# Performance work log

Hardware: AMD Instinct MI355X
Metric: run time of the kernel (lower is better)

## Reference

```python
import jax, jax.numpy as jnp
import numpy as np

B, S, D = 2, 512, 2048          # batch, seq, hidden
H, Dh = 16, 128                 # heads, head_dim
E, K, G, TG = 8, 2, 2, 1        # experts, top_k, n_group, topk_group
I, IS = 1024, 1024              # routed / shared expert intermediate
ROUTED_SCALE = 2.5
EPS = 1e-6
ROPE_THETA = 10000.0


def setup_inputs() -> dict:
    key = jax.random.key(0)
    ks = jax.random.split(key, 13)
    p = lambda k, shape, s=0.02: jax.random.normal(k, shape, jnp.float32) * s
    return {
        "hidden_states": jax.random.normal(ks[0], (B, S, D), jnp.float32),
        "ln1_w": jnp.ones((D,), jnp.float32),
        "ln2_w": jnp.ones((D,), jnp.float32),
        "wq": p(ks[1], (D, H * Dh)),
        "wk": p(ks[2], (D, H * Dh)),
        "wv": p(ks[3], (D, H * Dh)),
        "wo": p(ks[4], (H * Dh, D)),
        "gate_w": p(ks[5], (E, D)),
        "gate_bias": p(ks[6], (E,), 0.1),
        "w_gate": p(ks[7], (E, D, I)),
        "w_up": p(ks[8], (E, D, I)),
        "w_down": p(ks[9], (E, I, D)),
        "sw_gate": p(ks[10], (D, IS)),
        "sw_up": p(ks[11], (D, IS)),
        "sw_down": p(ks[12], (IS, D)),
    }


def _rmsnorm(x, w):
    var = jnp.mean(x * x, axis=-1, keepdims=True)
    return x * jax.lax.rsqrt(var + EPS) * w


def _rope_cos_sin(seq_len):
    inv_freq = 1.0 / (ROPE_THETA ** (jnp.arange(0, Dh, 2, dtype=jnp.float32) / Dh))
    ang = jnp.arange(seq_len, dtype=jnp.float32)[:, None] * inv_freq  # [S, Dh/2]
    return jnp.cos(ang)[None, :, None, :], jnp.sin(ang)[None, :, None, :]


def _apply_rope(x, cos, sin):
    x1, x2 = jnp.split(x, 2, axis=-1)
    return jnp.concatenate([x1 * cos - x2 * sin, x2 * cos + x1 * sin], axis=-1)


def _attention(x, wq, wk, wv, wo):
    q = (x @ wq).reshape(B, S, H, Dh)
    k = (x @ wk).reshape(B, S, H, Dh)
    v = (x @ wv).reshape(B, S, H, Dh)
    cos, sin = _rope_cos_sin(S)
    q = _apply_rope(q, cos, sin)
    k = _apply_rope(k, cos, sin)
    scores = jnp.einsum('bqhd,bkhd->bhqk', q, k) * (1.0 / np.sqrt(Dh).astype(np.float32))
    causal = jnp.tril(jnp.ones((S, S), bool))
    scores = jnp.where(causal, scores, jnp.finfo(scores.dtype).min)
    attn = jax.nn.softmax(scores, axis=-1)
    out = jnp.einsum('bhqk,bkhd->bqhd', attn, v).reshape(B, S, H * Dh)
    return out @ wo


def _moe(x, gate_w, gate_bias, w_gate, w_up, w_down, sw_gate, sw_up, sw_down):
    # x: [T, D]. noaux_tc grouped top-k routing (DeepSeek-V3 style).
    T = x.shape[0]
    logits = x @ gate_w.T                      # [T, E]
    scores = jax.nn.sigmoid(logits)
    sc = scores + gate_bias                    # selection scores with correction bias
    grp = sc.reshape(T, G, E // G)
    group_scores = jnp.sum(jax.lax.top_k(grp, 2)[0], axis=-1)  # top-2 sum per group [T,G]
    _, gidx = jax.lax.top_k(group_scores, TG)
    gmask = jnp.zeros((T, G), bool).at[jnp.arange(T)[:, None], gidx].set(True)
    emask = jnp.broadcast_to(gmask[:, :, None], (T, G, E // G)).reshape(T, E)
    masked = jnp.where(emask, sc, -jnp.inf)
    _, idx = jax.lax.top_k(masked, K)          # [T, K] expert ids
    w = jnp.take_along_axis(scores, idx, axis=-1)
    w = w / jnp.sum(w, axis=-1, keepdims=True)  # norm_topk_prob=True
    # dense combine weights [T, E] (zero except K entries per token)
    cw = jnp.zeros((T, E), x.dtype).at[jnp.arange(T)[:, None], idx].add(w)

    def body(acc, xs):
        wg, wu, wd, cwe = xs
        y = (jax.nn.silu(x @ wg) * (x @ wu)) @ wd  # SiluAndMul gated MLP
        return acc + cwe[:, None] * y, None

    routed, _ = jax.lax.scan(body, jnp.zeros_like(x), (w_gate, w_up, w_down, cw.T))
    shared = (jax.nn.silu(x @ sw_gate) * (x @ sw_up)) @ sw_down
    return routed * ROUTED_SCALE + shared


def reference(hidden_states, ln1_w, ln2_w, wq, wk, wv, wo, gate_w, gate_bias,
              w_gate, w_up, w_down, sw_gate, sw_up, sw_down):
    h = hidden_states
    h = h + _attention(_rmsnorm(h, ln1_w), wq, wk, wv, wo)
    x = _rmsnorm(h, ln2_w).reshape(B * S, D)
    moe_out = _moe(x, gate_w, gate_bias, w_gate, w_up, w_down,
                   sw_gate, sw_up, sw_down).reshape(B, S, D)
    return h + moe_out
```

## Files before the change

kernel.cpp:

```cpp
#include <hip/hip_runtime.h>

typedef __bf16 bf16x4 __attribute__((ext_vector_type(4)));
typedef __bf16 bf16x8 __attribute__((ext_vector_type(8)));
typedef float  f32x4  __attribute__((ext_vector_type(4)));

#define THREADS 256
constexpr int BK = 32, BKP = 40;

constexpr size_t MB = 1024*1024;
constexpr size_t oH2    = 0;
constexpr size_t oXB2   = 8*MB;
constexpr size_t oRT    = 12*MB;
constexpr size_t oWQKVT = 16*MB;
constexpr size_t oWQKVL = 40*MB;
constexpr size_t oWOT   = 64*MB;
constexpr size_t oWOL   = 72*MB;
constexpr size_t oXN1   = 80*MB;
constexpr size_t oXN1L  = 84*MB;
constexpr size_t oQKV   = 88*MB;
constexpr size_t oSCF   = 112*MB;
constexpr size_t oQKS   = 144*MB;
constexpr size_t oQKSL  = 152*MB;
constexpr size_t oVT    = 16*MB;
constexpr size_t oVTL   = 20*MB;
constexpr size_t oATT   = 24*MB;
constexpr size_t oPB    = 40*MB;
constexpr size_t oPBL2  = 88*MB;
constexpr size_t oWGUT  = 16*MB;
constexpr size_t oWDT   = 80*MB;
constexpr size_t oSGUT  = 112*MB;
constexpr size_t oSDT   = 120*MB;
constexpr size_t oGU    = 124*MB;
constexpr size_t oHB    = 140*MB;
constexpr size_t oY     = 144*MB;
constexpr size_t oSGU   = 16*MB;
constexpr size_t oSHB   = 24*MB;
constexpr size_t oSDB   = 26*MB;
constexpr size_t oEIDX = oRT;
constexpr size_t oEW   = oRT + 8192;
constexpr size_t oSLOT = oRT + 16384;
constexpr size_t oLIST = oRT + 24576;
constexpr size_t oCNT  = oRT + 32768;
constexpr size_t oOFF  = oRT + 33024;
constexpr size_t oCUR  = oRT + 33280;

__device__ __forceinline__ bf16x8 bzero8() {
  bf16x8 z;
#pragma unroll
  for (int j = 0; j < 8; ++j) z[j] = (__bf16)0.f;
  return z;
}

template<int OM>
__global__ void transpose_kernel(const float* __restrict__ in, __bf16* __restrict__ out,
                                 int ldin, int ldout, int zlo,
                                 long inBH, long inBL, long outB, long plane) {
  __shared__ float tile[64][65];
  int z = blockIdx.z;
  const float* inp = in + (long)(z / zlo) * inBH + (long)(z % zlo) * inBL;
  __bf16* outp = out + (long)z * outB;
  int r0 = blockIdx.y * 64, c0 = blockIdx.x * 64;
  int tid = threadIdx.x;
#pragma unroll
  for (int i = 0; i < 4; ++i) {
    int lin = tid + i * 256;
    int r = lin >> 4, c4 = (lin & 15) << 2;
    f32x4 v = *(const f32x4*)(inp + (long)(r0 + r) * ldin + c0 + c4);
    tile[r][c4] = v[0]; tile[r][c4+1] = v[1]; tile[r][c4+2] = v[2]; tile[r][c4+3] = v[3];
  }
  __syncthreads();
#pragma unroll
  for (int i = 0; i < 4; ++i) {
    int lin = tid + i * 256;
    int oR = lin >> 4, oC4 = (lin & 15) << 2;
    bf16x4 hi, lo;
#pragma unroll
    for (int j = 0; j < 4; ++j) {
      float v = tile[oC4 + j][oR];
      hi[j] = (__bf16)v;
      if constexpr (OM == 2) lo[j] = (__bf16)(v - (float)hi[j]);
    }
    __bf16* dst = outp + (long)(c0 + oR) * ldout + r0 + oC4;
    *(bf16x4*)dst = hi;
    if constexpr (OM == 2) *(bf16x4*)(dst + plane) = lo;
  }
}

template<int MODE, int SP, bool RESID, bool CAUSAL, bool KTRI, int TBM = 128, int TBN = 128>
__global__ __launch_bounds__(256, 2)
void gemm_kernel(const void* __restrict__ Av, const void* __restrict__ Bv, float* __restrict__ C,
                 const float* __restrict__ Rres,
                 int M, int N, int K, int lda, int ldb, int ldc,
                 int zlo, long aHi, long aLo, long bHi, long bLo, long cHi, long cLo,
                 long aPlane, long bPlane,
                 const int* __restrict__ counts, const int* __restrict__ offsets,
                 const int* __restrict__ gather) {
  const int n0 = blockIdx.x * TBN;
  const int m0 = blockIdx.y * TBM;
  const int z  = blockIdx.z;
  if (CAUSAL && n0 > m0) return;

  const float*  Af = (const float*)Av;
  const __bf16* Ah = (const __bf16*)Av;
  const __bf16* Bh = (const __bf16*)Bv;

  int mcount; int rowbase = 0;
  long aoff = 0, boff = 0, coff = 0;
  if constexpr (MODE == 0) {
    mcount = M;
    int zh = z / zlo, zl = z % zlo;
    aoff = (long)zh*aHi + (long)zl*aLo;
    boff = (long)zh*bHi + (long)zl*bLo;
    coff = (long)zh*cHi + (long)zl*cLo;
  } else {
    mcount = counts[z];
    rowbase = offsets[z];
    if (m0 >= mcount) return;
    boff = (long)z*bHi;
  }

  constexpr bool TRI = (SP != 0);
  constexpr int ABUF = TBM*BKP;
  constexpr int BBUF = TBN*BKP;
  constexpr int WTM = TBM/2, WTN = TBN/2;
  constexpr int MI = WTM/16, MJ = WTN/16;
  __shared__ __align__(16) __bf16 As[(TRI?2:1)*ABUF];
  __shared__ __align__(16) __bf16 Bs[(TRI?2:1)*BBUF];

  const int tid = threadIdx.x;
  const int lane = tid & 63, wave = tid >> 6;
  const int wm = wave >> 1, wn = wave & 1;
  const int lq = lane >> 4, lr = lane & 15;

  int kend = K;
  if (KTRI) { int ke = m0 + TBM; kend = ke < K ? ke : K; }

  f32x4 acc[MI][MJ] = {};

  for (int k0 = 0; k0 < kend; k0 += BK) {
    if (k0) __syncthreads();
    if constexpr (SP == 1) {
#pragma unroll
      for (int it = 0; it < TBM/32; ++it) {
        int lin = tid + it*THREADS;
        int row = lin >> 3;
        int c4  = (lin & 7) << 2;
        int gr  = m0 + row;
        bf16x4 hi, lo;
#pragma unroll
        for (int j = 0; j < 4; ++j) { hi[j]=(__bf16)0.f; lo[j]=(__bf16)0.f; }
        if (gr < mcount) {
          long arow = gr;
          f32x4 v = *(const f32x4*)(Af + aoff + arow*(long)lda + k0 + c4);
#pragma unroll
          for (int j = 0; j < 4; ++j) {
            hi[j] = (__bf16)v[j];
            lo[j] = (__bf16)(v[j] - (float)hi[j]);
          }
        }
        *(bf16x4*)(As + row*BKP + c4) = hi;
        *(bf16x4*)(As + ABUF + row*BKP + c4) = lo;
      }
    } else {
#pragma unroll
      for (int it = 0; it < TBM/64; ++it) {
        int lin = tid + it*THREADS;
        int row = lin >> 2;
        int c8  = (lin & 3) << 3;
        int gr  = m0 + row;
        bf16x8 hi = bzero8(), lo;
        if constexpr (SP == 2) lo = bzero8();
        if (gr < mcount) {
          long arow;
          if constexpr (MODE == 1) arow = gather[rowbase + gr];
          else if constexpr (MODE == 2) arow = rowbase + gr;
          else arow = gr;
          const __bf16* p = Ah + aoff + arow*(long)lda + k0 + c8;
          hi = *(const bf16x8*)p;
          if constexpr (SP == 2) lo = *(const bf16x8*)(p + aPlane);
        }
        *(bf16x8*)(As + row*BKP + c8) = hi;
        if constexpr (SP == 2) *(bf16x8*)(As + ABUF + row*BKP + c8) = lo;
      }
    }
#pragma unroll
    for (int it = 0; it < TBN/64; ++it) {
      int lin = tid + it*THREADS;
      int row = lin >> 2;
      int c8  = (lin & 3) << 3;
      const __bf16* p = Bh + boff + (long)(n0+row)*ldb + k0 + c8;
      *(bf16x8*)(Bs + row*BKP + c8) = *(const bf16x8*)p;
      if constexpr (TRI) *(bf16x8*)(Bs + BBUF + row*BKP + c8) = *(const bf16x8*)(p + bPlane);
    }
    __syncthreads();

    bf16x8 fa[MI], fal[MI];
    const __bf16* ap = As + (wm*WTM + lr)*BKP + lq*8;
    const __bf16* bp = Bs + (wn*WTN + lr)*BKP + lq*8;
#pragma unroll
    for (int i = 0; i < MI; ++i) {
      fa[i] = *(const bf16x8*)(ap + i*16*BKP);
      if constexpr (TRI) fal[i] = *(const bf16x8*)(ap + ABUF + i*16*BKP);
    }
#pragma unroll
    for (int j = 0; j < MJ; ++j) {
      bf16x8 fb = *(const bf16x8*)(bp + j*16*BKP);
      if constexpr (TRI) {
        bf16x8 fbl = *(const bf16x8*)(bp + BBUF + j*16*BKP);
#pragma unroll
        for (int i = 0; i < MI; ++i) {
          acc[i][j] = __builtin_amdgcn_mfma_f32_16x16x32_bf16(fa[i],  fbl, acc[i][j], 0, 0, 0);
          acc[i][j] = __builtin_amdgcn_mfma_f32_16x16x32_bf16(fal[i], fb,  acc[i][j], 0, 0, 0);
          acc[i][j] = __builtin_amdgcn_mfma_f32_16x16x32_bf16(fa[i],  fb,  acc[i][j], 0, 0, 0);
        }
      } else {
#pragma unroll
        for (int i = 0; i < MI; ++i)
          acc[i][j] = __builtin_amdgcn_mfma_f32_16x16x32_bf16(fa[i], fb, acc[i][j], 0, 0, 0);
      }
    }
  }

#pragma unroll
  for (int i = 0; i < MI; ++i) {
#pragma unroll
    for (int rg = 0; rg < 4; ++rg) {
      int lrow = wm*WTM + i*16 + lq*4 + rg;
      int gr = m0 + lrow;
      if (gr < mcount) {
        long crow = coff + (long)(rowbase + gr)*ldc;
#pragma unroll
        for (int j = 0; j < MJ; ++j) {
          int col = n0 + wn*WTN + j*16 + lr;
          float val = acc[i][j][rg];
          if constexpr (RESID) val += Rres[(long)gr*ldc + col];
          C[crow + col] = val;
        }
      }
    }
  }
}

template<int OM>
__global__ void rmsnorm_kernel(const float* __restrict__ x, const float* __restrict__ w,
                               __bf16* __restrict__ out, long plane) {
  const int row = blockIdx.x;
  const float* xr = x + (long)row * 2048;
  float ss = 0.f;
  for (int d = threadIdx.x; d < 2048; d += 256) { float v = xr[d]; ss += v*v; }
  __shared__ float red[4];
  int lane = threadIdx.x & 63, wave = threadIdx.x >> 6;
#pragma unroll
  for (int off = 32; off; off >>= 1) ss += __shfl_down(ss, off, 64);
  if (lane == 0) red[wave] = ss;
  __syncthreads();
  float tot = red[0] + red[1] + red[2] + red[3];
  float rs = rsqrtf(tot * (1.f/2048.f) + 1e-6f);
  __bf16* orow = out + (long)row * 2048;
  for (int d = threadIdx.x; d < 2048; d += 256) {
    float v = xr[d]*rs*w[d];
    __bf16 h = (__bf16)v;
    orow[d] = h;
    if constexpr (OM == 2) orow[d + plane] = (__bf16)(v - (float)h);
  }
}

__global__ void rope_split_kernel(const float* __restrict__ qkv, __bf16* __restrict__ o, long plane) {
  int tid = blockIdx.x*256 + threadIdx.x;
  int i = tid & 63;
  int th = tid >> 6;
  int h = th & 15;
  int t = th >> 4;
  int s = t & 511;
  long ib = (long)t*6144 + h*128;
  long ob = (long)t*4096 + h*128;
  float inv = 1.f / powf(10000.f, (float)i * (1.f/64.f));
  float ang = (float)s * inv;
  float c = cosf(ang), sn = sinf(ang);
  float q1 = qkv[ib+i], q2 = qkv[ib+64+i];
  float r1 = q1*c - q2*sn, r2 = q2*c + q1*sn;
  __bf16 h1 = (__bf16)r1, h2v = (__bf16)r2;
  o[ob+i] = h1;            o[ob+i+plane] = (__bf16)(r1 - (float)h1);
  o[ob+64+i] = h2v;        o[ob+64+i+plane] = (__bf16)(r2 - (float)h2v);
  float k1 = qkv[ib+2048+i], k2 = qkv[ib+2048+64+i];
  float s1 = k1*c - k2*sn, s2 = k2*c + k1*sn;
  __bf16 g1 = (__bf16)s1, g2 = (__bf16)s2;
  o[ob+2048+i] = g1;       o[ob+2048+i+plane] = (__bf16)(s1 - (float)g1);
  o[ob+2048+64+i] = g2;    o[ob+2048+64+i+plane] = (__bf16)(s2 - (float)g2);
}

__global__ void softmax_kernel(const float* __restrict__ sc, __bf16* __restrict__ p, long plane) {
  int r = blockIdx.x & 511;
  long bh = blockIdx.x >> 9;
  const float scale = 0.08838834764831845f;
  long base = (bh*512 + r)*512;
  int c0 = threadIdx.x, c1 = threadIdx.x + 256;
  float v0 = (c0 <= r) ? sc[base+c0]*scale : -3.0e38f;
  float v1 = (c1 <= r) ? sc[base+c1]*scale : -3.0e38f;
  float m = fmaxf(v0, v1);
  __shared__ float red[4];
  int lane = threadIdx.x & 63, wave = threadIdx.x >> 6;
#pragma unroll
  for (int off = 32; off; off >>= 1) m = fmaxf(m, __shfl_xor(m, off, 64));
  if (lane == 0) red[wave] = m;
  __syncthreads();
  m = fmaxf(fmaxf(red[0], red[1]), fmaxf(red[2], red[3]));
  __syncthreads();
  float e0 = (c0 <= r) ? expf(v0 - m) : 0.f;
  float e1 = (c1 <= r) ? expf(v1 - m) : 0.f;
  float s = e0 + e1;
#pragma unroll
  for (int off = 32; off; off >>= 1) s += __shfl_xor(s, off, 64);
  if (lane == 0) red[wave] = s;
  __syncthreads();
  s = red[0] + red[1] + red[2] + red[3];
  float inv = 1.f / s;
  float p0 = e0*inv, p1 = e1*inv;
  __bf16 h0 = (__bf16)p0, h1 = (__bf16)p1;
  p[base+c0] = h0; p[base+c0+plane] = (__bf16)(p0 - (float)h0);
  p[base+c1] = h1; p[base+c1+plane] = (__bf16)(p1 - (float)h1);
}

__global__ void zero8_kernel(int* c) { if (threadIdx.x < 8) c[threadIdx.x] = 0; }

__global__ void routing_kernel(const float* __restrict__ h2, const float* __restrict__ ln2w,
                               const float* __restrict__ gw, const float* __restrict__ gb,
                               int* __restrict__ eidx, float* __restrict__ ew,
                               int* __restrict__ counts) {
  int t = blockIdx.x;
  const float* xr = h2 + (long)t*2048;
  int lane = threadIdx.x & 63, wave = threadIdx.x >> 6;
  float ss = 0.f;
  for (int d = threadIdx.x; d < 2048; d += 256) { float v = xr[d]; ss += v*v; }
  __shared__ float red[4];
#pragma unroll
  for (int off = 32; off; off >>= 1) ss += __shfl_down(ss, off, 64);
  if (lane == 0) red[wave] = ss;
  __syncthreads();
  float rs = rsqrtf((red[0]+red[1]+red[2]+red[3]) * (1.f/2048.f) + 1e-6f);
  __shared__ float lg[8];
  for (int e = wave; e < 8; e += 4) {
    const float* wr = gw + (long)e*2048;
    float acc = 0.f;
    for (int d = lane; d < 2048; d += 64) acc += (xr[d]*rs*ln2w[d]) * wr[d];
#pragma unroll
    for (int off = 32; off; off >>= 1) acc += __shfl_down(acc, off, 64);
    if (lane == 0) lg[e] = acc;
  }
  __syncthreads();
  if (threadIdx.x == 0) {
    float sg[8], sc[8];
#pragma unroll
    for (int e = 0; e < 8; ++e) { sg[e] = 1.f/(1.f+expf(-lg[e])); sc[e] = sg[e] + gb[e]; }
    float gs[2];
#pragma unroll
    for (int g = 0; g < 2; ++g) {
      float m1 = -3e38f, m2 = -3e38f;
#pragma unroll
      for (int j = 0; j < 4; ++j) {
        float v = sc[4*g+j];
        if (v > m1) { m2 = m1; m1 = v; } else if (v > m2) m2 = v;
      }
      gs[g] = m1 + m2;
    }
    int b4 = (gs[1] > gs[0]) ? 4 : 0;
    int i1 = 0; float v1 = -3e38f;
#pragma unroll
    for (int j = 0; j < 4; ++j) if (sc[b4+j] > v1) { v1 = sc[b4+j]; i1 = j; }
    int i2 = -1; float v2 = -3e38f;
#pragma unroll
    for (int j = 0; j < 4; ++j) if (j != i1 && sc[b4+j] > v2) { v2 = sc[b4+j]; i2 = j; }
    float w1 = sg[b4+i1], w2 = sg[b4+i2], s = w1 + w2;
    eidx[t*2] = b4+i1; eidx[t*2+1] = b4+i2;
    ew[t*2] = w1/s;    ew[t*2+1] = w2/s;
    atomicAdd(&counts[b4+i1], 1); atomicAdd(&counts[b4+i2], 1);
  }
}

__global__ void scan_kernel(const int* __restrict__ counts, int* __restrict__ offsets,
                            int* __restrict__ cursors) {
  if (threadIdx.x == 0 && blockIdx.x == 0) {
    int s = 0;
    for (int e = 0; e < 8; ++e) { offsets[e] = s; s += counts[e]; cursors[e] = 0; }
    offsets[8] = s;
  }
}

__global__ void scatter_kernel(const int* __restrict__ eidx, const int* __restrict__ offsets,
                               int* __restrict__ cursors, int* __restrict__ list,
                               int* __restrict__ slot) {
  int t = blockIdx.x*256 + threadIdx.x;
  if (t < 1024) {
#pragma unroll
    for (int kk = 0; kk < 2; ++kk) {
      int e = eidx[t*2+kk];
      int pos = atomicAdd(&cursors[e], 1);
      int g = offsets[e] + pos;
      list[g] = t;
      slot[t*2+kk] = g;
    }
  }
}

__global__ void silumul_kernel(const float* __restrict__ gu, __bf16* __restrict__ o, int n) {
  int i = blockIdx.x*256 + threadIdx.x;
  if (i < n) {
    int s = i >> 10, j = i & 1023;
    float gv = gu[(long)s*2048 + j];
    float uv = gu[(long)s*2048 + 1024 + j];
    float sg = gv / (1.f + expf(-gv));
    o[i] = (__bf16)(sg * uv);
  }
}

__global__ void combine_kernel(const float* __restrict__ h2, const float* __restrict__ y,
                               const float* __restrict__ sdown, const int* __restrict__ slot,
                               const float* __restrict__ ew, float* __restrict__ out) {
  int i = blockIdx.x*256 + threadIdx.x;
  int t = i >> 11;
  int d = i & 2047;
  float rv = ew[t*2]   * y[(long)slot[t*2]  *2048 + d]
           + ew[t*2+1] * y[(long)slot[t*2+1]*2048 + d];
  out[i] = h2[i] + sdown[i] + 2.5f * rv;
}

extern "C" void kernel_launch(void* const* d_in, const int* in_sizes, int n_in,
                              void* d_out, int out_size, void* d_ws, size_t ws_size,
                              hipStream_t stream) {
  const float* hid  = (const float*)d_in[0];
  const float* ln1  = (const float*)d_in[1];
  const float* ln2  = (const float*)d_in[2];
  const float* wq   = (const float*)d_in[3];
  const float* wk   = (const float*)d_in[4];
  const float* wv   = (const float*)d_in[5];
  const float* wo   = (const float*)d_in[6];
  const float* gw   = (const float*)d_in[7];
  const float* gb   = (const float*)d_in[8];
  const float* wgat = (const float*)d_in[9];
  const float* wup  = (const float*)d_in[10];
  const float* wdn  = (const float*)d_in[11];
  const float* swg  = (const float*)d_in[12];
  const float* swu  = (const float*)d_in[13];
  const float* swd  = (const float*)d_in[14];
  float* out = (float*)d_out;
  char* ws = (char*)d_ws;

  float*  h2    = (float*)(ws + oH2);
  __bf16* xb2   = (__bf16*)(ws + oXB2);
  __bf16* wqkvT = (__bf16*)(ws + oWQKVT);
  __bf16* woT   = (__bf16*)(ws + oWOT);
  __bf16* xn1   = (__bf16*)(ws + oXN1);
  float*  qkv   = (float*)(ws + oQKV);
  float*  scf   = (float*)(ws + oSCF);
  __bf16* qks   = (__bf16*)(ws + oQKS);
  __bf16* vtb   = (__bf16*)(ws + oVT);
  float*  att   = (float*)(ws + oATT);
  __bf16* pb    = (__bf16*)(ws + oPB);
  __bf16* wgut  = (__bf16*)(ws + oWGUT);
  __bf16* wdt   = (__bf16*)(ws + oWDT);
  __bf16* sgut  = (__bf16*)(ws + oSGUT);
  __bf16* sdt   = (__bf16*)(ws + oSDT);
  float*  gu    = (float*)(ws + oGU);
  __bf16* hb    = (__bf16*)(ws + oHB);
  float*  ybuf  = (float*)(ws + oY);
  float*  sgu   = (float*)(ws + oSGU);
  __bf16* shb   = (__bf16*)(ws + oSHB);
  float*  sdb   = (float*)(ws + oSDB);
  int*   eidx = (int*)(ws + oEIDX);
  float* ew   = (float*)(ws + oEW);
  int*   slot = (int*)(ws + oSLOT);
  int*   list = (int*)(ws + oLIST);
  int*   cnt  = (int*)(ws + oCNT);
  int*   offs = (int*)(ws + oOFF);
  int*   curs = (int*)(ws + oCUR);

  const long S22 = (long)2048*2048, S21 = (long)2048*1024;
  const long pWQKV = (oWQKVL - oWQKVT) / 2;
  const long pWO   = (oWOL - oWOT) / 2;
  const long pXN1  = 2*MB;
  const long pQKS  = (oQKSL - oQKS) / 2;
  const long pVT   = 2*MB;
  const long pPB   = (oPBL2 - oPB) / 2;

  transpose_kernel<2><<<dim3(32,32,1), 256, 0, stream>>>(wq, wqkvT,          2048, 2048, 1, 0, 0, 0, pWQKV);
  transpose_kernel<2><<<dim3(32,32,1), 256, 0, stream>>>(wk, wqkvT + S22,    2048, 2048, 1, 0, 0, 0, pWQKV);
  transpose_kernel<2><<<dim3(32,32,1), 256, 0, stream>>>(wv, wqkvT + 2*S22,  2048, 2048, 1, 0, 0, 0, pWQKV);
  transpose_kernel<2><<<dim3(32,32,1), 256, 0, stream>>>(wo, woT,            2048, 2048, 1, 0, 0, 0, pWO);

  rmsnorm_kernel<2><<<1024, 256, 0, stream>>>(hid, ln1, xn1, pXN1);

  gemm_kernel<0, 2, false, false, false, 64, 128><<<dim3(48,16,1), 256, 0, stream>>>(
      xn1, wqkvT, qkv, nullptr, 1024, 6144, 2048, 2048, 2048, 6144,
      1, 0, 0, 0, 0, 0, 0, pXN1, pWQKV, nullptr, nullptr, nullptr);

  rope_split_kernel<<<4096, 256, 0, stream>>>(qkv, qks, pQKS);

  transpose_kernel<2><<<dim3(2,8,32), 256, 0, stream>>>(
      qkv + 4096, vtb, 6144, 512, 16, (long)512*6144, 128, (long)128*512, pVT);

  gemm_kernel<0, 2, false, true, false, 64, 64><<<dim3(8,8,32), 256, 0, stream>>>(
      qks, qks + 2048, scf, nullptr, 512, 512, 128, 4096, 4096, 512,
      16, (long)512*4096, 128, (long)512*4096, 128, (long)16*512*512, (long)512*512,
      pQKS, pQKS, nullptr, nullptr, nullptr);

  softmax_kernel<<<16384, 256, 0, stream>>>(scf, pb, pPB);

  gemm_kernel<0, 2, false, false, true, 64, 64><<<dim3(2,8,32), 256, 0, stream>>>(
      pb, vtb, att, nullptr, 512, 128, 512, 512, 512, 2048,
      16, (long)16*512*512, (long)512*512, (long)16*128*512, (long)128*512,
      (long)512*2048, 128, pPB, pVT, nullptr, nullptr, nullptr);

  gemm_kernel<0, 1, true, false, false, 64, 64><<<dim3(32,16,1), 256, 0, stream>>>(
      att, woT, h2, hid, 1024, 2048, 2048, 2048, 2048, 2048,
      1, 0, 0, 0, 0, 0, 0, 0, pWO, nullptr, nullptr, nullptr);

  rmsnorm_kernel<1><<<1024, 256, 0, stream>>>(h2, ln2, xb2, 0);
  zero8_kernel<<<1, 64, 0, stream>>>(cnt);
  routing_kernel<<<1024, 256, 0, stream>>>(h2, ln2, gw, gb, eidx, ew, cnt);
  scan_kernel<<<1, 64, 0, stream>>>(cnt, offs, curs);
  scatter_kernel<<<4, 256, 0, stream>>>(eidx, offs, curs, list, slot);

  transpose_kernel<1><<<dim3(16,32,8), 256, 0, stream>>>(wgat, wgut,        1024, 2048, 1, S21, 0, S22, 0);
  transpose_kernel<1><<<dim3(16,32,8), 256, 0, stream>>>(wup,  wgut + S21,  1024, 2048, 1, S21, 0, S22, 0);
  transpose_kernel<1><<<dim3(32,16,8), 256, 0, stream>>>(wdn,  wdt,         2048, 1024, 1, S21, 0, S21, 0);
  transpose_kernel<1><<<dim3(16,32,1), 256, 0, stream>>>(swg,  sgut,        1024, 2048, 1, 0, 0, 0, 0);
  transpose_kernel<1><<<dim3(16,32,1), 256, 0, stream>>>(swu,  sgut + S21,  1024, 2048, 1, 0, 0, 0, 0);
  transpose_kernel<1><<<dim3(32,16,1), 256, 0, stream>>>(swd,  sdt,         2048, 1024, 1, 0, 0, 0, 0);

  gemm_kernel<1, 0, false, false, false, 64, 64><<<dim3(32,16,8), 256, 0, stream>>>(
      xb2, wgut, gu, nullptr, 1024, 2048, 2048, 2048, 2048, 2048,
      1, 0, 0, S22, 0, 0, 0, 0, 0, cnt, offs, list);
  silumul_kernel<<<8192, 256, 0, stream>>>(gu, hb, 2048*1024);
  gemm_kernel<2, 0, false, false, false, 64, 64><<<dim3(32,16,8), 256, 0, stream>>>(
      hb, wdt, ybuf, nullptr, 1024, 2048, 1024, 1024, 1024, 2048,
      1, 0, 0, S21, 0, 0, 0, 0, 0, cnt, offs, nullptr);

  gemm_kernel<0, 0, false, false, false, 64, 64><<<dim3(32,16,1), 256, 0, stream>>>(
      xb2, sgut, sgu, nullptr, 1024, 2048, 2048, 2048, 2048, 2048,
      1, 0, 0, 0, 0, 0, 0, 0, 0, nullptr, nullptr, nullptr);
  silumul_kernel<<<4096, 256, 0, stream>>>(sgu, shb, 1024*1024);
  gemm_kernel<0, 0, false, false, false, 64, 64><<<dim3(32,16,1), 256, 0, stream>>>(
      shb, sdt, sdb, nullptr, 1024, 2048, 1024, 1024, 1024, 2048,
      1, 0, 0, 0, 0, 0, 0, 0, 0, nullptr, nullptr, nullptr);

  combine_kernel<<<8192, 256, 0, stream>>>(h2, ybuf, sdb, slot, ew, out);
}
```

Baseline: 812.7 us.

## Double-buffer GEMM shared tiles with register prefetch of next K slice

```diff
diff --git a/kernel.cpp b/kernel.cpp
--- a/kernel.cpp
+++ b/kernel.cpp
@@ -122,10 +122,12 @@
   constexpr bool TRI = (SP != 0);
   constexpr int ABUF = TBM*BKP;
   constexpr int BBUF = TBN*BKP;
+  constexpr int ASZ = (TRI?2:1)*ABUF;
+  constexpr int BSZ = (TRI?2:1)*BBUF;
   constexpr int WTM = TBM/2, WTN = TBN/2;
   constexpr int MI = WTM/16, MJ = WTN/16;
-  __shared__ __align__(16) __bf16 As[(TRI?2:1)*ABUF];
-  __shared__ __align__(16) __bf16 Bs[(TRI?2:1)*BBUF];
+  __shared__ __align__(16) __bf16 As[2*ASZ];
+  __shared__ __align__(16) __bf16 Bs[2*BSZ];
 
   const int tid = threadIdx.x;
   const int lane = tid & 63, wave = tid >> 6;
@@ -137,66 +139,101 @@
 
   f32x4 acc[MI][MJ] = {};
 
-  for (int k0 = 0; k0 < kend; k0 += BK) {
-    if (k0) __syncthreads();
+  constexpr int NAF = (SP==1) ? TBM/32 : 1;
+  constexpr int NAH = (SP!=1) ? TBM/64 : 1;
+  constexpr int NB  = TBN/64;
+  f32x4  arf[NAF];
+  bf16x8 arh[NAH], arl[NAH];
+  bf16x8 brh[NB],  brl[NB];
+
+  auto loadAB = [&](int kk) {
     if constexpr (SP == 1) {
 #pragma unroll
-      for (int it = 0; it < TBM/32; ++it) {
+      for (int it = 0; it < NAF; ++it) {
         int lin = tid + it*THREADS;
-        int row = lin >> 3;
-        int c4  = (lin & 7) << 2;
-        int gr  = m0 + row;
-        bf16x4 hi, lo;
-#pragma unroll
-        for (int j = 0; j < 4; ++j) { hi[j]=(__bf16)0.f; lo[j]=(__bf16)0.f; }
-        if (gr < mcount) {
-          long arow = gr;
-          f32x4 v = *(const f32x4*)(Af + aoff + arow*(long)lda + k0 + c4);
-#pragma unroll
-          for (int j = 0; j < 4; ++j) {
-            hi[j] = (__bf16)v[j];
-            lo[j] = (__bf16)(v[j] - (float)hi[j]);
-          }
-        }
-        *(bf16x4*)(As + row*BKP + c4) = hi;
-        *(bf16x4*)(As + ABUF + row*BKP + c4) = lo;
+        int row = lin >> 3, c4 = (lin & 7) << 2;
+        int gr = m0 + row;
+        f32x4 zv; zv[0]=0.f; zv[1]=0.f; zv[2]=0.f; zv[3]=0.f;
+        arf[it] = (gr < mcount) ? *(const f32x4*)(Af + aoff + (long)gr*lda + kk + c4) : zv;
       }
     } else {
 #pragma unroll
-      for (int it = 0; it < TBM/64; ++it) {
+      for (int it = 0; it < NAH; ++it) {
         int lin = tid + it*THREADS;
-        int row = lin >> 2;
-        int c8  = (lin & 3) << 3;
-        int gr  = m0 + row;
-        bf16x8 hi = bzero8(), lo;
-        if constexpr (SP == 2) lo = bzero8();
+        int row = lin >> 2, c8 = (lin & 3) << 3;
+        int gr = m0 + row;
+        arh[it] = bzero8();
+        if constexpr (SP == 2) arl[it] = bzero8();
         if (gr < mcount) {
           long arow;
           if constexpr (MODE == 1) arow = gather[rowbase + gr];
           else if constexpr (MODE == 2) arow = rowbase + gr;
           else arow = gr;
-          const __bf16* p = Ah + aoff + arow*(long)lda + k0 + c8;
-          hi = *(const bf16x8*)p;
-          if constexpr (SP == 2) lo = *(const bf16x8*)(p + aPlane);
+          const __bf16* p = Ah + aoff + arow*(long)lda + kk + c8;
+          arh[it] = *(const bf16x8*)p;
+          if constexpr (SP == 2) arl[it] = *(const bf16x8*)(p + aPlane);
         }
-        *(bf16x8*)(As + row*BKP + c8) = hi;
-        if constexpr (SP == 2) *(bf16x8*)(As + ABUF + row*BKP + c8) = lo;
-      }
-    }
-#pragma unroll
-    for (int it = 0; it < TBN/64; ++it) {
+      }
+    }
+#pragma unroll
+    for (int it = 0; it < NB; ++it) {
       int lin = tid + it*THREADS;
-      int row = lin >> 2;
-      int c8  = (lin & 3) << 3;
-      const __bf16* p = Bh + boff + (long)(n0+row)*ldb + k0 + c8;
-      *(bf16x8*)(Bs + row*BKP + c8) = *(const bf16x8*)p;
-      if constexpr (TRI) *(bf16x8*)(Bs + BBUF + row*BKP + c8) = *(const bf16x8*)(p + bPlane);
-    }
-    __syncthreads();
-
+      int row = lin >> 2, c8 = (lin & 3) << 3;
+      const __bf16* p = Bh + boff + (long)(n0+row)*ldb + kk + c8;
+      brh[it] = *(const bf16x8*)p;
+      if constexpr (TRI) brl[it] = *(const bf16x8*)(p + bPlane);
+    }
+  };
+
+  auto writeAB = [&](int b) {
+    __bf16* Ad = As + b*ASZ;
+    __bf16* Bd = Bs + b*BSZ;
+    if constexpr (SP == 1) {
+#pragma unroll
+      for (int it = 0; it < NAF; ++it) {
+        int lin = tid + it*THREADS;
+        int row = lin >> 3, c4 = (lin & 7) << 2;
+        bf16x4 hi, lo;
+#pragma unroll
+        for (int j = 0; j < 4; ++j) {
+          hi[j] = (__bf16)arf[it][j];
+          lo[j] = (__bf16)(arf[it][j] - (float)hi[j]);
+        }
+        *(bf16x4*)(Ad + row*BKP + c4) = hi;
+        *(bf16x4*)(Ad + ABUF + row*BKP + c4) = lo;
+      }
+    } else {
+#pragma unroll
+      for (int it = 0; it < NAH; ++it) {
+        int lin = tid + it*THREADS;
+        int row = lin >> 2, c8 = (lin & 3) << 3;
+        *(bf16x8*)(Ad + row*BKP + c8) = arh[it];
+        if constexpr (SP == 2) *(bf16x8*)(Ad + ABUF + row*BKP + c8) = arl[it];
+      }
+    }
+#pragma unroll
+    for (int it = 0; it < NB; ++it) {
+      int lin = tid + it*THREADS;
+      int row = lin >> 2, c8 = (lin & 3) << 3;
+      *(bf16x8*)(Bd + row*BKP + c8) = brh[it];
+      if constexpr (TRI) *(bf16x8*)(Bd + BBUF + row*BKP + c8) = brl[it];
+    }
+  };
+
+  loadAB(0);
+  writeAB(0);
+  __syncthreads();
+  int cur = 0;
+
+  for (int k0 = 0; k0 < kend; k0 += BK) {
+    const bool hn = (k0 + BK < kend);
+    if (hn) loadAB(k0 + BK);
+
+    const __bf16* Ab = As + cur*ASZ;
+    const __bf16* Bb = Bs + cur*BSZ;
     bf16x8 fa[MI], fal[MI];
-    const __bf16* ap = As + (wm*WTM + lr)*BKP + lq*8;
-    const __bf16* bp = Bs + (wn*WTN + lr)*BKP + lq*8;
+    const __bf16* ap = Ab + (wm*WTM + lr)*BKP + lq*8;
+    const __bf16* bp = Bb + (wn*WTN + lr)*BKP + lq*8;
 #pragma unroll
     for (int i = 0; i < MI; ++i) {
       fa[i] = *(const bf16x8*)(ap + i*16*BKP);
@@ -218,6 +255,12 @@
         for (int i = 0; i < MI; ++i)
           acc[i][j] = __builtin_amdgcn_mfma_f32_16x16x32_bf16(fa[i], fb, acc[i][j], 0, 0, 0);
       }
+    }
+
+    if (hn) {
+      writeAB(cur ^ 1);
+      __syncthreads();
+      cur ^= 1;
     }
   }
 
```

Measured after the change: 784.8 us. 3.4% less time.
